# Kernel optimization log

Measured on AMD Instinct MI355X. Metric: run time of the kernel, lower is better.

## Reference

```python
import jax, jax.numpy as jnp
import numpy as np

B, C, D = 16384, 4096, 256

def setup_inputs() -> dict:
    key = jax.random.key(0)
    k1, k2, k3 = jax.random.split(key, 3)
    z = jax.random.normal(k1, (B, D), dtype=jnp.float32)
    mu = jax.random.normal(k2, (C, D), dtype=jnp.float32)
    logvar = jax.random.normal(k3, (C, D), dtype=jnp.float32)
    return {"z": z, "mu": mu, "logvar": logvar}

def reference(z, mu, logvar):
    # Vectorized form of the per-class loop in _approx_class_probabilities.
    # log_gauss(z; mu_c, logvar_c) = -0.5*(sum_d((z-mu_c)^2/var_c + logvar_c) + D*log(2pi))
    # Expand (z-mu)^2/var = z^2/var - 2*z*mu/var + mu^2/var so the sum over d
    # becomes three [B,D]x[D,C] contractions (no [B,C,D] intermediate).
    d = z.shape[1]
    num_classes = mu.shape[0]
    log_prior = jnp.float32(np.log(1.0 / num_classes))
    inv_var = jnp.exp(-logvar)                                   # [C, D]
    quad = (jnp.einsum('bd,cd->bc', z * z, inv_var)
            - 2.0 * jnp.einsum('bd,cd->bc', z, mu * inv_var)
            + jnp.sum(mu * mu * inv_var, axis=1)[None, :])       # [B, C]
    logvar_sum = jnp.sum(logvar, axis=1)[None, :]                # [1, C]
    class_logits = -0.5 * (quad + logvar_sum + d * jnp.float32(np.log(2 * np.pi))) + log_prior
    class_prob = jax.nn.softmax(class_logits, axis=1)
    predicted_classes = jnp.argmax(class_prob, axis=1)
    return class_logits, class_prob, predicted_classes
```

## Files before the change

kernel.cpp:

```cpp
#include <hip/hip_runtime.h>
#include <math.h>


constexpr int M = 16384;
constexpr int N = 4096;
constexpr int DD = 256;
constexpr int K = 1536;
constexpr int BM = 128, BN = 128, BK = 64;

typedef _Float16 half_t;
typedef __attribute__((ext_vector_type(8))) _Float16 half8;
typedef __attribute__((ext_vector_type(4))) float floatx4;

#define GLOBAL_AS(p) ((const __attribute__((address_space(1))) void*)(p))
#define LDS_AS(p) ((__attribute__((address_space(3))) void*)(p))

__global__ __launch_bounds__(256) void prep_w_kernel(const float* __restrict__ mu,
                                                     const float* __restrict__ logvar,
                                                     half_t* __restrict__ Wt,
                                                     float* __restrict__ Kc) {
    const int c = blockIdx.x;
    const int d = threadIdx.x;
    const float lv = logvar[(size_t)c * DD + d];
    const float m  = mu[(size_t)c * DD + d];
    const float iv = __expf(-lv);
    const float w1 = -0.5f * iv;
    const float w2 = m * iv;
    const half_t w1h = (half_t)w1;
    const half_t w1l = (half_t)(w1 - (float)w1h);
    const half_t w2h = (half_t)w2;
    const half_t w2l = (half_t)(w2 - (float)w2h);
    half_t* row = Wt + (size_t)c * K;
    row[d]        = w1h;
    row[256 + d]  = w2h;
    row[512 + d]  = w1l;
    row[768 + d]  = w2l;
    row[1024 + d] = w1h;
    row[1280 + d] = w2h;

    float s = m * m * iv + lv;
    #pragma unroll
    for (int off = 32; off > 0; off >>= 1) s += __shfl_down(s, off, 64);
    __shared__ float ls[4];
    const int lane = threadIdx.x & 63, wvi = threadIdx.x >> 6;
    if (lane == 0) ls[wvi] = s;
    __syncthreads();
    if (threadIdx.x == 0) {
        const float t = ls[0] + ls[1] + ls[2] + ls[3];
        Kc[c] = -0.5f * t - 235.24826450039618f - 8.31776616671934f;
    }
}

__global__ __launch_bounds__(256) void prep_a_kernel(const float* __restrict__ z,
                                                     half_t* __restrict__ At) {
    const int b = blockIdx.x;
    const int d = threadIdx.x;
    const float zv = z[(size_t)b * DD + d];
    const float z2 = zv * zv;
    const half_t z2h = (half_t)z2;
    const half_t z2l = (half_t)(z2 - (float)z2h);
    const half_t zh  = (half_t)zv;
    const half_t zl  = (half_t)(zv - (float)zh);
    half_t* row = At + (size_t)b * K;
    row[d]        = z2h;
    row[256 + d]  = zh;
    row[512 + d]  = z2h;
    row[768 + d]  = zh;
    row[1024 + d] = z2l;
    row[1280 + d] = zl;
}

__global__ __launch_bounds__(256) void gemm_kernel(const half_t* __restrict__ At,
                                                   const half_t* __restrict__ Wt,
                                                   const float* __restrict__ Kc,
                                                   float* __restrict__ logits) {
    __shared__ half_t As[BM * BK];
    __shared__ half_t Bs[BN * BK];

    const int bn0 = blockIdx.x * BN;
    const int bm0 = blockIdx.y * BM;
    const int tid = threadIdx.x;
    const int lane = tid & 63;
    const int wvi = tid >> 6;
    const int wm = (wvi & 1) * 64;
    const int wn = (wvi >> 1) * 64;
    const int quad = lane >> 4;
    const int l15 = lane & 15;

    const int r0 = tid >> 3;
    const int cl = ((tid & 7) ^ (r0 & 7)) * 8;
    const char* gA = (const char*)(At + (size_t)(bm0 + r0) * K + cl);
    const char* gB = (const char*)(Wt + (size_t)(bn0 + r0) * K + cl);
    char* lA = (char*)As + tid * 16;
    char* lB = (char*)Bs + tid * 16;

    floatx4 acc[4][4] = {};

    for (int kt = 0; kt < K / BK; ++kt) {
        const size_t kb = (size_t)kt * BK * 2;
        #pragma unroll
        for (int i = 0; i < 4; ++i) {
            __builtin_amdgcn_global_load_lds(GLOBAL_AS(gA + kb + (size_t)i * 32 * K * 2),
                                             LDS_AS(lA + i * 4096), 16, 0, 0);
            __builtin_amdgcn_global_load_lds(GLOBAL_AS(gB + kb + (size_t)i * 32 * K * 2),
                                             LDS_AS(lB + i * 4096), 16, 0, 0);
        }
        __syncthreads();
        #pragma unroll
        for (int ks = 0; ks < 2; ++ks) {
            half8 af[4], bf[4];
            #pragma unroll
            for (int mi = 0; mi < 4; ++mi) {
                const int m = wm + mi * 16 + l15;
                const int c8 = (ks * 4 + quad) ^ (m & 7);
                af[mi] = *(const half8*)(As + m * BK + c8 * 8);
            }
            #pragma unroll
            for (int ni = 0; ni < 4; ++ni) {
                const int n = wn + ni * 16 + l15;
                const int c8 = (ks * 4 + quad) ^ (n & 7);
                bf[ni] = *(const half8*)(Bs + n * BK + c8 * 8);
            }
            #pragma unroll
            for (int mi = 0; mi < 4; ++mi)
                #pragma unroll
                for (int ni = 0; ni < 4; ++ni)
                    acc[mi][ni] = __builtin_amdgcn_mfma_f32_16x16x32_f16(
                        af[mi], bf[ni], acc[mi][ni], 0, 0, 0);
        }
        __syncthreads();
    }

    float kc[4];
    #pragma unroll
    for (int ni = 0; ni < 4; ++ni) kc[ni] = Kc[bn0 + wn + ni * 16 + l15];
    #pragma unroll
    for (int mi = 0; mi < 4; ++mi) {
        const int row0 = bm0 + wm + mi * 16 + quad * 4;
        #pragma unroll
        for (int ni = 0; ni < 4; ++ni) {
            const int col = bn0 + wn + ni * 16 + l15;
            float* outp = logits + (size_t)row0 * N + col;
            #pragma unroll
            for (int r = 0; r < 4; ++r)
                outp[(size_t)r * N] = acc[mi][ni][r] + kc[ni];
        }
    }
}

__global__ __launch_bounds__(256) void softmax_kernel(const float* __restrict__ logits,
                                                      float* __restrict__ probs,
                                                      float* __restrict__ pred) {
    const int row = blockIdx.x;
    const int tid = threadIdx.x;
    const int lane = tid & 63, wvi = tid >> 6;
    const float4* lrow = (const float4*)(logits + (size_t)row * N);
    float4 v[4];
    float vmax = -INFINITY;
    int vidx = 0;
    #pragma unroll
    for (int j = 0; j < 4; ++j) {
        v[j] = lrow[j * 256 + tid];
        const int base = (j * 256 + tid) * 4;
        if (v[j].x > vmax) { vmax = v[j].x; vidx = base; }
        if (v[j].y > vmax) { vmax = v[j].y; vidx = base + 1; }
        if (v[j].z > vmax) { vmax = v[j].z; vidx = base + 2; }
        if (v[j].w > vmax) { vmax = v[j].w; vidx = base + 3; }
    }
    #pragma unroll
    for (int off = 32; off > 0; off >>= 1) {
        const float ov = __shfl_down(vmax, off, 64);
        const int oi = __shfl_down(vidx, off, 64);
        if (ov > vmax || (ov == vmax && oi < vidx)) { vmax = ov; vidx = oi; }
    }
    __shared__ float smax[4];
    __shared__ int sidx[4];
    __shared__ float ssum[4];
    if (lane == 0) { smax[wvi] = vmax; sidx[wvi] = vidx; }
    __syncthreads();
    float rmax = smax[0];
    int ridx = sidx[0];
    #pragma unroll
    for (int i = 1; i < 4; ++i)
        if (smax[i] > rmax || (smax[i] == rmax && sidx[i] < ridx)) { rmax = smax[i]; ridx = sidx[i]; }

    float s = 0.f;
    float4 e[4];
    #pragma unroll
    for (int j = 0; j < 4; ++j) {
        e[j].x = __expf(v[j].x - rmax);
        e[j].y = __expf(v[j].y - rmax);
        e[j].z = __expf(v[j].z - rmax);
        e[j].w = __expf(v[j].w - rmax);
        s += e[j].x + e[j].y + e[j].z + e[j].w;
    }
    #pragma unroll
    for (int off = 32; off > 0; off >>= 1) s += __shfl_down(s, off, 64);
    if (lane == 0) ssum[wvi] = s;
    __syncthreads();
    const float inv = 1.f / (ssum[0] + ssum[1] + ssum[2] + ssum[3]);
    float4* prow = (float4*)(probs + (size_t)row * N);
    #pragma unroll
    for (int j = 0; j < 4; ++j) {
        float4 o;
        o.x = e[j].x * inv; o.y = e[j].y * inv; o.z = e[j].z * inv; o.w = e[j].w * inv;
        prow[j * 256 + tid] = o;
    }
    if (tid == 0) pred[row] = (float)ridx;
}

extern "C" void kernel_launch(void* const* d_in, const int* in_sizes, int n_in,
                              void* d_out, int out_size, void* d_ws, size_t ws_size,
                              hipStream_t stream) {
    const float* z      = (const float*)d_in[0];
    const float* mu     = (const float*)d_in[1];
    const float* logvar = (const float*)d_in[2];
    float* out    = (float*)d_out;
    float* logits = out;
    float* probs  = out + (size_t)M * N;
    float* pred   = out + (size_t)2 * M * N;

    char* scratch = (char*)probs;
    half_t* At = (half_t*)scratch;
    half_t* Wt = (half_t*)(scratch + (size_t)M * K * 2);
    float*  Kc = (float*)(scratch + (size_t)M * K * 2 + (size_t)N * K * 2);

    prep_w_kernel<<<N, 256, 0, stream>>>(mu, logvar, Wt, Kc);
    prep_a_kernel<<<M, 256, 0, stream>>>(z, At);
    gemm_kernel<<<dim3(N / BN, M / BM), 256, 0, stream>>>(At, Wt, Kc, logits);
    softmax_kernel<<<M, 256, 0, stream>>>(logits, probs, pred);
}
```

Baseline: 784.6 us.

## Double-buffer GEMM with 256x256 tiles, 8 waves, and XCD-aware block mapping

Restructures the GEMM so each 512-thread block computes a 256x256 tile, and staggers global-to-LDS loads of the next A tile and the B tile two steps ahead into a double buffer. The loads are interleaved with MFMA phases under explicit waitcnt, barriers and setprio. It also remaps the 1D block id so blocks on the same XCD share B column tiles for L2 reuse. The aim is to hide load latency and raise arithmetic intensity. The cost is more registers and LDS per block and fragile hand-written synchronisation.

```diff
diff --git a/kernel.cpp b/kernel.cpp
--- a/kernel.cpp
+++ b/kernel.cpp
@@ -6,7 +6,8 @@
 constexpr int N = 4096;
 constexpr int DD = 256;
 constexpr int K = 1536;
-constexpr int BM = 128, BN = 128, BK = 64;
+constexpr int BM = 256, BN = 256, BK = 64;
+constexpr int NT = K / BK;
 
 typedef _Float16 half_t;
 typedef __attribute__((ext_vector_type(8))) _Float16 half8;
@@ -70,20 +71,24 @@
     row[1280 + d] = zl;
 }
 
-__global__ __launch_bounds__(256) void gemm_kernel(const half_t* __restrict__ At,
-                                                   const half_t* __restrict__ Wt,
-                                                   const float* __restrict__ Kc,
-                                                   float* __restrict__ logits) {
-    __shared__ half_t As[BM * BK];
-    __shared__ half_t Bs[BN * BK];
-
-    const int bn0 = blockIdx.x * BN;
-    const int bm0 = blockIdx.y * BM;
+__global__ __launch_bounds__(512, 2) void gemm_kernel(const half_t* __restrict__ At,
+                                                      const half_t* __restrict__ Wt,
+                                                      const float* __restrict__ Kc,
+                                                      float* __restrict__ logits) {
+    __shared__ half_t As[2][BM * BK];
+    __shared__ half_t Bs[2][BN * BK];
+
+    const int bid = blockIdx.x;
+    const int xcd = bid & 7;
+    const int lid = bid >> 3;
+    const int bn0 = (xcd * 2 + (lid & 1)) * BN;
+    const int bm0 = (lid >> 1) * BM;
+
     const int tid = threadIdx.x;
     const int lane = tid & 63;
     const int wvi = tid >> 6;
-    const int wm = (wvi & 1) * 64;
-    const int wn = (wvi >> 1) * 64;
+    const int wm = (wvi >> 2) * 128;
+    const int wn = (wvi & 3) * 64;
     const int quad = lane >> 4;
     const int l15 = lane & 15;
 
@@ -94,48 +99,87 @@
     char* lA = (char*)As + tid * 16;
     char* lB = (char*)Bs + tid * 16;
 
-    floatx4 acc[4][4] = {};
-
-    for (int kt = 0; kt < K / BK; ++kt) {
-        const size_t kb = (size_t)kt * BK * 2;
+    #define STAGE(g, l, kt, h, buf)                                             \
+        _Pragma("unroll")                                                       \
+        for (int jj = 0; jj < 2; ++jj) {                                        \
+            const int j = (h) * 2 + jj;                                         \
+            __builtin_amdgcn_global_load_lds(                                   \
+                GLOBAL_AS((g) + (size_t)(kt) * BK * 2 + (size_t)j * 64 * K * 2),\
+                LDS_AS((l) + (buf) * 32768 + j * 8192), 16, 0, 0);              \
+        }
+
+    floatx4 acc[8][4] = {};
+
+    STAGE(gA, lA, 0, 0, 0); STAGE(gA, lA, 0, 1, 0);
+    STAGE(gB, lB, 0, 0, 0); STAGE(gB, lB, 0, 1, 0);
+    STAGE(gB, lB, 1, 0, 1); STAGE(gB, lB, 1, 1, 1);
+    asm volatile("s_waitcnt vmcnt(4)" ::: "memory");
+    __builtin_amdgcn_s_barrier();
+    asm volatile("" ::: "memory");
+
+    for (int t = 0; t < NT; ++t) {
+        const int p = t & 1;
+        const half_t* Ab = &As[p][0];
+        const half_t* Bb = &Bs[p][0];
+        half8 bf[8];
         #pragma unroll
-        for (int i = 0; i < 4; ++i) {
-            __builtin_amdgcn_global_load_lds(GLOBAL_AS(gA + kb + (size_t)i * 32 * K * 2),
-                                             LDS_AS(lA + i * 4096), 16, 0, 0);
-            __builtin_amdgcn_global_load_lds(GLOBAL_AS(gB + kb + (size_t)i * 32 * K * 2),
-                                             LDS_AS(lB + i * 4096), 16, 0, 0);
+        for (int q = 0; q < 4; ++q) {
+            half8 af[4];
+            #pragma unroll
+            for (int ii = 0; ii < 2; ++ii) {
+                const int m = wm + (2 * q + ii) * 16 + l15;
+                #pragma unroll
+                for (int ks = 0; ks < 2; ++ks) {
+                    const int c8 = (ks * 4 + quad) ^ (m & 7);
+                    af[ii * 2 + ks] = *(const half8*)(Ab + m * BK + c8 * 8);
+                }
+            }
+            if (q == 0) {
+                #pragma unroll
+                for (int ni = 0; ni < 4; ++ni) {
+                    const int n = wn + ni * 16 + l15;
+                    #pragma unroll
+                    for (int ks = 0; ks < 2; ++ks) {
+                        const int c8 = (ks * 4 + quad) ^ (n & 7);
+                        bf[ni * 2 + ks] = *(const half8*)(Bb + n * BK + c8 * 8);
+                    }
+                }
+            }
+            if (q < 2) {
+                if (t + 1 < NT) STAGE(gA, lA, t + 1, q, p ^ 1);
+            } else {
+                if (t + 2 < NT) STAGE(gB, lB, t + 2, q - 2, p);
+            }
+            __builtin_amdgcn_s_barrier();
+            asm volatile("s_waitcnt lgkmcnt(0)" ::: "memory");
+            __builtin_amdgcn_sched_barrier(0);
+            __builtin_amdgcn_s_setprio(1);
+            #pragma unroll
+            for (int ks = 0; ks < 2; ++ks)
+                #pragma unroll
+                for (int ii = 0; ii < 2; ++ii)
+                    #pragma unroll
+                    for (int ni = 0; ni < 4; ++ni)
+                        acc[2 * q + ii][ni] = __builtin_amdgcn_mfma_f32_16x16x32_f16(
+                            af[ii * 2 + ks], bf[ni * 2 + ks], acc[2 * q + ii][ni], 0, 0, 0);
+            __builtin_amdgcn_s_setprio(0);
+            if (q == 3) {
+                if (t + 2 < NT) {
+                    asm volatile("s_waitcnt vmcnt(4)" ::: "memory");
+                } else if (t + 1 < NT) {
+                    asm volatile("s_waitcnt vmcnt(0)" ::: "memory");
+                }
+            }
+            __builtin_amdgcn_s_barrier();
+            asm volatile("" ::: "memory");
         }
-        __syncthreads();
-        #pragma unroll
-        for (int ks = 0; ks < 2; ++ks) {
-            half8 af[4], bf[4];
-            #pragma unroll
-            for (int mi = 0; mi < 4; ++mi) {
-                const int m = wm + mi * 16 + l15;
-                const int c8 = (ks * 4 + quad) ^ (m & 7);
-                af[mi] = *(const half8*)(As + m * BK + c8 * 8);
-            }
-            #pragma unroll
-            for (int ni = 0; ni < 4; ++ni) {
-                const int n = wn + ni * 16 + l15;
-                const int c8 = (ks * 4 + quad) ^ (n & 7);
-                bf[ni] = *(const half8*)(Bs + n * BK + c8 * 8);
-            }
-            #pragma unroll
-            for (int mi = 0; mi < 4; ++mi)
-                #pragma unroll
-                for (int ni = 0; ni < 4; ++ni)
-                    acc[mi][ni] = __builtin_amdgcn_mfma_f32_16x16x32_f16(
-                        af[mi], bf[ni], acc[mi][ni], 0, 0, 0);
-        }
-        __syncthreads();
     }
 
     float kc[4];
     #pragma unroll
     for (int ni = 0; ni < 4; ++ni) kc[ni] = Kc[bn0 + wn + ni * 16 + l15];
     #pragma unroll
-    for (int mi = 0; mi < 4; ++mi) {
+    for (int mi = 0; mi < 8; ++mi) {
         const int row0 = bm0 + wm + mi * 16 + quad * 4;
         #pragma unroll
         for (int ni = 0; ni < 4; ++ni) {
@@ -146,6 +190,7 @@
                 outp[(size_t)r * N] = acc[mi][ni][r] + kc[ni];
         }
     }
+    #undef STAGE
 }
 
 __global__ __launch_bounds__(256) void softmax_kernel(const float* __restrict__ logits,
@@ -227,6 +272,6 @@
 
     prep_w_kernel<<<N, 256, 0, stream>>>(mu, logvar, Wt, Kc);
     prep_a_kernel<<<M, 256, 0, stream>>>(z, At);
-    gemm_kernel<<<dim3(N / BN, M / BM), 256, 0, stream>>>(At, Wt, Kc, logits);
+    gemm_kernel<<<dim3(N / BN * M / BM), 512, 0, stream>>>(At, Wt, Kc, logits);
     softmax_kernel<<<M, 256, 0, stream>>>(logits, probs, pred);
 }
```

Result: slower. 818.0 us (+4.2%).
